# Optimization experiments

Hardware: AMD Instinct MI355X
Metric: run time of the kernel (lower is better)

## Reference

```python
import jax, jax.numpy as jnp
import numpy as np

B, C, H, W = 2, 512, 30, 40
K = 64
PATCH, STRIDE = 4, 1
EPS = 1e-12  # torch F.normalize eps


def _l2norm(v, axis):
    n = jnp.sqrt(jnp.sum(v * v, axis=axis, keepdims=True))
    return v / jnp.maximum(n, EPS)


def setup_inputs() -> dict:
    key = jax.random.key(0)
    k1, k2, k3 = jax.random.split(key, 3)
    x = jax.random.normal(k1, (B, C, H, W), dtype=jnp.float32)
    conv_w = jax.random.normal(k2, (K, C), dtype=jnp.float32) * 0.05  # 1x1 conv weight, no bias (vlad_v2=False)
    centroids = jax.random.normal(k3, (K, C), dtype=jnp.float32)
    return {"x": x, "conv_w": conv_w, "centroids": centroids}


def reference(x, conv_w, centroids):
    b, c, h, w = x.shape
    k = centroids.shape[0]
    # input L2 normalization along channels
    xn = _l2norm(x, axis=1)
    # soft assignment: 1x1 conv + softmax over clusters
    soft = jax.nn.softmax(jnp.einsum('kc,bchw->bkhw', conv_w, xn), axis=1)
    # weighted residuals [B,K,C,H,W] (fused; original loops over K)
    resid = (xn[:, None, :, :, :] - centroids[None, :, :, None, None]) * soft[:, :, None, :, :]
    # global VLAD: sum over spatial
    vlad_global = jnp.sum(resid, axis=(-2, -1))  # [B,K,C]
    vlad_global = _l2norm(vlad_global, axis=2).reshape(b, -1)
    vlad_global = _l2norm(vlad_global, axis=1)
    # integral image over [B, K*C, H, W]
    r = resid.reshape(b, k * c, h, w)
    integ = jnp.cumsum(jnp.cumsum(r, axis=-1), axis=-2)
    integ = jnp.pad(integ, ((0, 0), (0, 0), (1, 0), (1, 0)))  # [B,KC,H+1,W+1]
    # box-sum via integral-image differences (equiv. to the dilated 2x2 grouped conv)
    p, s = PATCH, STRIDE
    hp = (h - p) // s + 1
    wp = (w - p) // s + 1
    ye, xe = (hp - 1) * s + 1, (wp - 1) * s + 1
    tl = integ[:, :, 0:ye:s, 0:xe:s]
    tr = integ[:, :, 0:ye:s, p:p + xe:s]
    bl = integ[:, :, p:p + ye:s, 0:xe:s]
    br = integ[:, :, p:p + ye:s, p:p + xe:s]
    box = (br - tr - bl + tl) / (p * p)  # [B,KC,hp,wp]
    v = box.reshape(b, k, c, hp * wp)
    v = _l2norm(v, axis=2)  # intra-cluster norm
    v = v.reshape(b, k * c, hp * wp)
    vlad_local = _l2norm(v, axis=1)  # [B, K*C, hp*wp]
    return (vlad_local, vlad_global)
```

## Files before the change

### kernel.cpp

```cpp
#include <hip/hip_runtime.h>
#include <math.h>

#define BB 2
#define CC 512
#define HH 30
#define WW 40
#define KK 64
#define NPIX (HH*WW)
#define HP 27
#define WP 37
#define NP (HP*WP)
#define LEPS 1e-12f
#define NCG 16

__global__ __launch_bounds__(512) void k_norm_soft(
    const float* __restrict__ x, const float* __restrict__ convw,
    float* __restrict__ xn, float* __restrict__ soft)
{
  const int h = blockIdx.x, b = blockIdx.y;
  const int t = threadIdx.x;
  __shared__ float xc[64][41];
  __shared__ float cw[64][65];
  __shared__ float Lb[KK][WW + 1];
  __shared__ float psum[12][WW];
  __shared__ float invn[WW];
  __shared__ float mx[WW], Zs[WW];

  const size_t xbase = (size_t)b * CC * NPIX + (size_t)h * WW;

  if (t < 480) {
    const int w = t % 40, part = t / 40;
    float s = 0.f;
    for (int c = part; c < CC; c += 12) {
      const float v = x[xbase + (size_t)c * NPIX + w];
      s = fmaf(v, v, s);
    }
    psum[part][w] = s;
  }
  __syncthreads();
  if (t < 40) {
    float s = 0.f;
    #pragma unroll
    for (int p = 0; p < 12; ++p) s += psum[p][t];
    invn[t] = 1.f / fmaxf(sqrtf(s), LEPS);
  }
  __syncthreads();

  const int k = t & 63, wp = t >> 6;
  float acc[5] = {0.f, 0.f, 0.f, 0.f, 0.f};
  for (int cb = 0; cb < CC; cb += 64) {
    #pragma unroll
    for (int n = 0; n < 5; ++n) {
      const int idx = t + 512 * n;
      const int c = idx / 40, w = idx % 40;
      const float v = x[xbase + (size_t)(cb + c) * NPIX + w] * invn[w];
      xc[c][w] = v;
      xn[xbase + (size_t)(cb + c) * NPIX + w] = v;
    }
    #pragma unroll
    for (int n = 0; n < 8; ++n) {
      const int idx = t + 512 * n;
      const int kk2 = idx >> 6, c2 = idx & 63;
      cw[kk2][c2] = convw[(size_t)kk2 * CC + cb + c2];
    }
    __syncthreads();
    #pragma unroll 1
    for (int c = 0; c < 64; ++c) {
      const float cv = cw[k][c];
      #pragma unroll
      for (int n = 0; n < 5; ++n)
        acc[n] = fmaf(cv, xc[c][wp + 8 * n], acc[n]);
    }
    __syncthreads();
  }
  #pragma unroll
  for (int n = 0; n < 5; ++n) Lb[k][wp + 8 * n] = acc[n];
  __syncthreads();
  if (t < 40) {
    float m = -1e30f;
    for (int kk2 = 0; kk2 < KK; ++kk2) m = fmaxf(m, Lb[kk2][t]);
    float Z = 0.f;
    for (int kk2 = 0; kk2 < KK; ++kk2) Z += expf(Lb[kk2][t] - m);
    mx[t] = m; Zs[t] = Z;
  }
  __syncthreads();
  const size_t sbase = (size_t)b * KK * NPIX + (size_t)h * WW;
  #pragma unroll
  for (int n = 0; n < 5; ++n) {
    const int idx = t + 512 * n;
    const int kk2 = idx / 40, w = idx % 40;
    soft[sbase + (size_t)kk2 * NPIX + w] = expf(Lb[kk2][w] - mx[w]) / Zs[w];
  }
}

__global__ __launch_bounds__(256) void k_global(
    const float* __restrict__ xn, const float* __restrict__ soft,
    const float* __restrict__ cent, float* __restrict__ ghat)
{
  const int k = blockIdx.x, b = blockIdx.y, t = threadIdx.x;
  __shared__ float sb[NPIX];
  __shared__ float red[256];
  const float* srow = soft + ((size_t)b * KK + k) * NPIX;
  for (int i2 = t; i2 < NPIX; i2 += 256) sb[i2] = srow[i2];
  __syncthreads();
  float p = 0.f;
  for (int i2 = t; i2 < NPIX; i2 += 256) p += sb[i2];
  red[t] = p;
  __syncthreads();
  for (int s = 128; s > 0; s >>= 1) { if (t < s) red[t] += red[t + s]; __syncthreads(); }
  const float Sg = red[0];
  __syncthreads();

  const int c0 = t, c1 = t + 256;
  const float* x0 = xn + ((size_t)b * CC + c0) * NPIX;
  const float* x1 = xn + ((size_t)b * CC + c1) * NPIX;
  float a0 = 0.f, a1 = 0.f;
  for (int p4 = 0; p4 < NPIX; p4 += 4) {
    const float4 s4 = *(const float4*)&sb[p4];
    const float4 v0 = *(const float4*)(x0 + p4);
    const float4 v1 = *(const float4*)(x1 + p4);
    a0 = fmaf(s4.x, v0.x, a0); a0 = fmaf(s4.y, v0.y, a0);
    a0 = fmaf(s4.z, v0.z, a0); a0 = fmaf(s4.w, v0.w, a0);
    a1 = fmaf(s4.x, v1.x, a1); a1 = fmaf(s4.y, v1.y, a1);
    a1 = fmaf(s4.z, v1.z, a1); a1 = fmaf(s4.w, v1.w, a1);
  }
  const float g0 = a0 - cent[(size_t)k * CC + c0] * Sg;
  const float g1 = a1 - cent[(size_t)k * CC + c1] * Sg;
  red[t] = g0 * g0 + g1 * g1;
  __syncthreads();
  for (int s = 128; s > 0; s >>= 1) { if (t < s) red[t] += red[t + s]; __syncthreads(); }
  const float inv = 1.f / fmaxf(sqrtf(red[0]), LEPS);
  float* gr = ghat + ((size_t)b * KK + k) * CC;
  gr[c0] = g0 * inv; gr[c1] = g1 * inv;
}

__global__ __launch_bounds__(256) void k_global2(
    const float* __restrict__ ghat, float* __restrict__ outg)
{
  const int b = blockIdx.x, t = threadIdx.x;
  __shared__ float red[256];
  const float* gb = ghat + (size_t)b * KK * CC;
  float p = 0.f;
  for (int i2 = t; i2 < KK * CC; i2 += 256) { const float v = gb[i2]; p = fmaf(v, v, p); }
  red[t] = p;
  __syncthreads();
  for (int s = 128; s > 0; s >>= 1) { if (t < s) red[t] += red[t + s]; __syncthreads(); }
  const float inv = 1.f / fmaxf(sqrtf(red[0]), LEPS);
  for (int i2 = t; i2 < KK * CC; i2 += 256)
    outg[(size_t)b * KK * CC + i2] = gb[i2] * inv;
}

template<int PHASE>
__global__ __launch_bounds__(320, 3) void k_local4(
    const float* __restrict__ xn, const float* __restrict__ soft,
    const float* __restrict__ cent, float* __restrict__ sp,
    const float* __restrict__ fs, float* __restrict__ out)
{
  const int cg = blockIdx.x;
  const int kg = blockIdx.y;
  const int bz = blockIdx.z;
  const int b = bz / 7, iq = bz % 7;
  const int i0 = iq * 4;
  const int n_i = (iq == 6) ? 3 : 4;
  const int k0 = kg * 4, c0 = cg * 32;
  const int t = threadIdx.x;

  __shared__ float xn_l[32][280];
  __shared__ float soft_l[4][280];
  __shared__ float cent_l[4][32];

  for (int u = t; u < 2240; u += 320) {
    const int c = u / 70, rem = u % 70;
    const int rl = rem / 10, q = rem % 10;
    int row = i0 + rl; if (row > HH - 1) row = HH - 1;
    *(float4*)&xn_l[c][rl * 40 + q * 4] =
      *(const float4*)&xn[((size_t)(b * CC + c0 + c)) * NPIX + (size_t)row * 40 + q * 4];
  }
  if (t < 280) {
    const int kk = t / 70, rem = t % 70;
    const int rl = rem / 10, q = rem % 10;
    int row = i0 + rl; if (row > HH - 1) row = HH - 1;
    *(float4*)&soft_l[kk][rl * 40 + q * 4] =
      *(const float4*)&soft[((size_t)(b * KK + k0 + kk)) * NPIX + (size_t)row * 40 + q * 4];
  }
  if (t < 128) cent_l[t >> 5][t & 31] = cent[(size_t)(k0 + (t >> 5)) * CC + c0 + (t & 31)];
  __syncthreads();

  const int c8 = (PHASE == 0) ? (t & 7) : (t / 40);
  const int j  = (PHASE == 0) ? (t >> 3) : (t % 40);

  for (int ii = 0; ii < n_i; ++ii) {
    const int i = i0 + ii;
    float acc[4][4];
    float Ssum[4] = {0.f, 0.f, 0.f, 0.f};
    #pragma unroll
    for (int cc = 0; cc < 4; ++cc)
      #pragma unroll
      for (int kk = 0; kk < 4; ++kk) acc[cc][kk] = 0.f;

    #pragma unroll
    for (int r = 0; r < 4; ++r) {
      const int base = (ii + r) * 40 + j;
      float sv[4][4], xv[4][4];
      #pragma unroll
      for (int kk = 0; kk < 4; ++kk)
        #pragma unroll
        for (int dx = 0; dx < 4; ++dx) sv[kk][dx] = soft_l[kk][base + dx];
      #pragma unroll
      for (int cc = 0; cc < 4; ++cc)
        #pragma unroll
        for (int dx = 0; dx < 4; ++dx) xv[cc][dx] = xn_l[cc * 8 + c8][base + dx];
      #pragma unroll
      for (int kk = 0; kk < 4; ++kk)
        Ssum[kk] += (sv[kk][0] + sv[kk][1]) + (sv[kk][2] + sv[kk][3]);
      #pragma unroll
      for (int cc = 0; cc < 4; ++cc)
        #pragma unroll
        for (int kk = 0; kk < 4; ++kk) {
          float a = acc[cc][kk];
          a = fmaf(xv[cc][0], sv[kk][0], a);
          a = fmaf(xv[cc][1], sv[kk][1], a);
          a = fmaf(xv[cc][2], sv[kk][2], a);
          a = fmaf(xv[cc][3], sv[kk][3], a);
          acc[cc][kk] = a;
        }
    }

    if (PHASE == 0) {
      #pragma unroll
      for (int kk = 0; kk < 4; ++kk) {
        float s = 0.f;
        #pragma unroll
        for (int cc = 0; cc < 4; ++cc) {
          const float raw = fmaf(-cent_l[kk][cc * 8 + c8], Ssum[kk], acc[cc][kk]);
          s = fmaf(raw, raw, s);
        }
        s += __shfl_xor(s, 1, 64);
        s += __shfl_xor(s, 2, 64);
        s += __shfl_xor(s, 4, 64);
        if (c8 == 0 && j < WP)
          sp[(((size_t)(b * KK + k0 + kk)) * NCG + cg) * NP + (size_t)i * WP + j] = s;
      }
    } else if (j < WP) {
      float fsv[4];
      #pragma unroll
      for (int kk = 0; kk < 4; ++kk)
        fsv[kk] = fs[((size_t)(b * KK + k0 + kk)) * NP + (size_t)i * WP + j];
      #pragma unroll
      for (int kk = 0; kk < 4; ++kk)
        #pragma unroll
        for (int cc = 0; cc < 4; ++cc) {
          const float raw = fmaf(-cent_l[kk][cc * 8 + c8], Ssum[kk], acc[cc][kk]);
          out[((size_t)((b * KK + k0 + kk) * CC + c0 + cc * 8 + c8)) * NP
              + (size_t)i * WP + j] = raw * fsv[kk];
        }
    }
  }
}

__global__ __launch_bounds__(256) void k_nf(
    const float* __restrict__ sp, float* __restrict__ fs)
{
  const int b = blockIdx.y, t = threadIdx.x;
  const int k = t >> 2, dp = t & 3;
  const int p = blockIdx.x * 4 + dp;
  __shared__ float red[64][4];
  __shared__ float inv2s[4];
  const bool ok = p < NP;
  float sr = 0.f;
  if (ok) {
    #pragma unroll
    for (int g = 0; g < NCG; ++g)
      sr += sp[(((size_t)(b * KK + k)) * NCG + g) * NP + p];
  }
  const float iv = 1.f / fmaxf(sqrtf(sr) * 0.0625f, LEPS);
  red[k][dp] = sr * (1.f / 256.f) * iv * iv;
  __syncthreads();
  if (t < 4) {
    float s = 0.f;
    #pragma unroll
    for (int kk = 0; kk < 64; ++kk) s += red[kk][t];
    inv2s[t] = 1.f / fmaxf(sqrtf(s), LEPS);
  }
  __syncthreads();
  if (ok)
    fs[((size_t)(b * KK + k)) * NP + p] = 0.0625f * iv * inv2s[dp];
}

extern "C" void kernel_launch(void* const* d_in, const int* in_sizes, int n_in,
                              void* d_out, int out_size, void* d_ws, size_t ws_size,
                              hipStream_t stream)
{
  const float* x     = (const float*)d_in[0];
  const float* convw = (const float*)d_in[1];
  const float* cent  = (const float*)d_in[2];
  float* out = (float*)d_out;
  float* ws  = (float*)d_ws;

  float* xn   = ws;
  float* soft = xn   + (size_t)BB * CC * NPIX;
  float* fs   = soft + (size_t)BB * KK * NPIX;
  float* ghat = fs   + (size_t)BB * KK * NP;
  float* sp   = ghat + (size_t)BB * KK * CC;

  k_norm_soft<<<dim3(HH, BB), 512, 0, stream>>>(x, convw, xn, soft);
  k_global<<<dim3(KK, BB), 256, 0, stream>>>(xn, soft, cent, ghat);
  k_global2<<<dim3(BB), 256, 0, stream>>>(ghat, out + (size_t)BB * KK * CC * NP);
  k_local4<0><<<dim3(NCG, KK / 4, BB * 7), 320, 0, stream>>>(xn, soft, cent, sp, fs, out);
  k_nf<<<dim3((NP + 3) / 4, BB), 256, 0, stream>>>(sp, fs);
  k_local4<1><<<dim3(NCG, KK / 4, BB * 7), 320, 0, stream>>>(xn, soft, cent, sp, fs, out);
}
```

Before: 442.3 us.

## Register-block local box-sum kernel over 4 output columns and split global norm

The local VLAD kernel is restructured so each thread computes a 4-wide strip of output columns for one row, using float4 shared-memory loads with a padded row stride. This reuses loaded x and soft values across the overlapping 4x4 windows. The soft-assignment window sums are now computed once per block into shared memory instead of being recomputed by every channel thread. The single-block global L2 normalization is split into a reduction kernel and a grid-wide scaling kernel, which spreads the 32K-element write across many blocks. The cost is higher register pressure (64 accumulators per thread), and the PHASE 1 stores become strided per thread, which may reduce write coalescing.

```diff
diff --git a/kernel.cpp b/kernel.cpp
--- a/kernel.cpp
+++ b/kernel.cpp
@@ -12,6 +12,7 @@
 #define NP (HP*WP)
 #define LEPS 1e-12f
 #define NCG 16
+#define XSTR 292
 
 __global__ __launch_bounds__(512) void k_norm_soft(
     const float* __restrict__ x, const float* __restrict__ convw,
@@ -134,8 +135,8 @@
   gr[c0] = g0 * inv; gr[c1] = g1 * inv;
 }
 
-__global__ __launch_bounds__(256) void k_global2(
-    const float* __restrict__ ghat, float* __restrict__ outg)
+__global__ __launch_bounds__(256) void k_g2a(
+    const float* __restrict__ ghat, float* __restrict__ inv2g)
 {
   const int b = blockIdx.x, t = threadIdx.x;
   __shared__ float red[256];
@@ -145,13 +146,21 @@
   red[t] = p;
   __syncthreads();
   for (int s = 128; s > 0; s >>= 1) { if (t < s) red[t] += red[t + s]; __syncthreads(); }
-  const float inv = 1.f / fmaxf(sqrtf(red[0]), LEPS);
-  for (int i2 = t; i2 < KK * CC; i2 += 256)
-    outg[(size_t)b * KK * CC + i2] = gb[i2] * inv;
+  if (t == 0) inv2g[b] = 1.f / fmaxf(sqrtf(red[0]), LEPS);
+}
+
+__global__ __launch_bounds__(256) void k_g2b(
+    const float* __restrict__ ghat, const float* __restrict__ inv2g,
+    float* __restrict__ outg)
+{
+  const int b = blockIdx.y;
+  const int u = blockIdx.x * 256 + threadIdx.x;
+  if (u < KK * CC)
+    outg[(size_t)b * KK * CC + u] = ghat[(size_t)b * KK * CC + u] * inv2g[b];
 }
 
 template<int PHASE>
-__global__ __launch_bounds__(320, 3) void k_local4(
+__global__ __launch_bounds__(320, 3) void k_local5(
     const float* __restrict__ xn, const float* __restrict__ soft,
     const float* __restrict__ cent, float* __restrict__ sp,
     const float* __restrict__ fs, float* __restrict__ out)
@@ -161,99 +170,137 @@
   const int bz = blockIdx.z;
   const int b = bz / 7, iq = bz % 7;
   const int i0 = iq * 4;
-  const int n_i = (iq == 6) ? 3 : 4;
   const int k0 = kg * 4, c0 = cg * 32;
   const int t = threadIdx.x;
-
-  __shared__ float xn_l[32][280];
-  __shared__ float soft_l[4][280];
+  const int c4 = t & 7;
+  const int jq = (t >> 3) % 10;
+  const int i2 = t / 80;
+  const int j0 = jq * 4;
+  const int i = i0 + i2;
+
+  __shared__ float xn_l[32 * XSTR];
+  __shared__ float soft_l[4 * XSTR];
+  __shared__ float S_l[4][4][48];
   __shared__ float cent_l[4][32];
 
   for (int u = t; u < 2240; u += 320) {
-    const int c = u / 70, rem = u % 70;
-    const int rl = rem / 10, q = rem % 10;
+    const int c = u / 70, rem = u - c * 70;
+    const int rl = rem / 10, q = rem - rl * 10;
     int row = i0 + rl; if (row > HH - 1) row = HH - 1;
-    *(float4*)&xn_l[c][rl * 40 + q * 4] =
+    *(float4*)&xn_l[c * XSTR + rl * 40 + q * 4] =
       *(const float4*)&xn[((size_t)(b * CC + c0 + c)) * NPIX + (size_t)row * 40 + q * 4];
   }
   if (t < 280) {
-    const int kk = t / 70, rem = t % 70;
-    const int rl = rem / 10, q = rem % 10;
+    const int kk = t / 70, rem = t - kk * 70;
+    const int rl = rem / 10, q = rem - rl * 10;
     int row = i0 + rl; if (row > HH - 1) row = HH - 1;
-    *(float4*)&soft_l[kk][rl * 40 + q * 4] =
+    *(float4*)&soft_l[kk * XSTR + rl * 40 + q * 4] =
       *(const float4*)&soft[((size_t)(b * KK + k0 + kk)) * NPIX + (size_t)row * 40 + q * 4];
   }
   if (t < 128) cent_l[t >> 5][t & 31] = cent[(size_t)(k0 + (t >> 5)) * CC + c0 + (t & 31)];
   __syncthreads();
 
-  const int c8 = (PHASE == 0) ? (t & 7) : (t / 40);
-  const int j  = (PHASE == 0) ? (t >> 3) : (t % 40);
-
-  for (int ii = 0; ii < n_i; ++ii) {
-    const int i = i0 + ii;
-    float acc[4][4];
-    float Ssum[4] = {0.f, 0.f, 0.f, 0.f};
-    #pragma unroll
-    for (int cc = 0; cc < 4; ++cc)
-      #pragma unroll
-      for (int kk = 0; kk < 4; ++kk) acc[cc][kk] = 0.f;
-
-    #pragma unroll
-    for (int r = 0; r < 4; ++r) {
-      const int base = (ii + r) * 40 + j;
-      float sv[4][4], xv[4][4];
+  if (t < 160) {
+    const int kk = t / 40, j = t - kk * 40;
+    #pragma unroll
+    for (int ii = 0; ii < 4; ++ii) {
+      float s = 0.f;
+      #pragma unroll
+      for (int r = 0; r < 4; ++r) {
+        const int base = kk * XSTR + (ii + r) * 40 + j;
+        s += (soft_l[base] + soft_l[base + 1]) + (soft_l[base + 2] + soft_l[base + 3]);
+      }
+      S_l[kk][ii][j] = s;
+    }
+  }
+  __syncthreads();
+
+  float acc[4][4][4];
+  #pragma unroll
+  for (int cc = 0; cc < 4; ++cc)
+    #pragma unroll
+    for (int kk = 0; kk < 4; ++kk)
+      #pragma unroll
+      for (int jd = 0; jd < 4; ++jd) acc[cc][kk][jd] = 0.f;
+
+  #pragma unroll
+  for (int r = 0; r < 4; ++r) {
+    const int rbase = (i2 + r) * 40 + j0;
+    float sw[4][8];
+    #pragma unroll
+    for (int kk = 0; kk < 4; ++kk) {
+      const float4 s0 = *(const float4*)&soft_l[kk * XSTR + rbase];
+      const float4 s1 = *(const float4*)&soft_l[kk * XSTR + rbase + 4];
+      sw[kk][0] = s0.x; sw[kk][1] = s0.y; sw[kk][2] = s0.z; sw[kk][3] = s0.w;
+      sw[kk][4] = s1.x; sw[kk][5] = s1.y; sw[kk][6] = s1.z; sw[kk][7] = s1.w;
+    }
+    #pragma unroll
+    for (int cc = 0; cc < 4; ++cc) {
+      const int cr = (cc * 8 + c4) * XSTR + rbase;
+      const float4 x0 = *(const float4*)&xn_l[cr];
+      const float4 x1 = *(const float4*)&xn_l[cr + 4];
+      const float xw[8] = {x0.x, x0.y, x0.z, x0.w, x1.x, x1.y, x1.z, x1.w};
       #pragma unroll
       for (int kk = 0; kk < 4; ++kk)
         #pragma unroll
-        for (int dx = 0; dx < 4; ++dx) sv[kk][dx] = soft_l[kk][base + dx];
-      #pragma unroll
-      for (int cc = 0; cc < 4; ++cc)
-        #pragma unroll
-        for (int dx = 0; dx < 4; ++dx) xv[cc][dx] = xn_l[cc * 8 + c8][base + dx];
-      #pragma unroll
-      for (int kk = 0; kk < 4; ++kk)
-        Ssum[kk] += (sv[kk][0] + sv[kk][1]) + (sv[kk][2] + sv[kk][3]);
-      #pragma unroll
-      for (int cc = 0; cc < 4; ++cc)
-        #pragma unroll
-        for (int kk = 0; kk < 4; ++kk) {
-          float a = acc[cc][kk];
-          a = fmaf(xv[cc][0], sv[kk][0], a);
-          a = fmaf(xv[cc][1], sv[kk][1], a);
-          a = fmaf(xv[cc][2], sv[kk][2], a);
-          a = fmaf(xv[cc][3], sv[kk][3], a);
-          acc[cc][kk] = a;
+        for (int jd = 0; jd < 4; ++jd) {
+          float a = acc[cc][kk][jd];
+          a = fmaf(xw[jd + 0], sw[kk][jd + 0], a);
+          a = fmaf(xw[jd + 1], sw[kk][jd + 1], a);
+          a = fmaf(xw[jd + 2], sw[kk][jd + 2], a);
+          a = fmaf(xw[jd + 3], sw[kk][jd + 3], a);
+          acc[cc][kk][jd] = a;
         }
     }
-
-    if (PHASE == 0) {
-      #pragma unroll
-      for (int kk = 0; kk < 4; ++kk) {
+  }
+
+  if (PHASE == 0) {
+    #pragma unroll
+    for (int kk = 0; kk < 4; ++kk) {
+      const float4 Sq = *(const float4*)&S_l[kk][i2][j0];
+      const float Sv[4] = {Sq.x, Sq.y, Sq.z, Sq.w};
+      float sq[4];
+      #pragma unroll
+      for (int jd = 0; jd < 4; ++jd) {
         float s = 0.f;
         #pragma unroll
         for (int cc = 0; cc < 4; ++cc) {
-          const float raw = fmaf(-cent_l[kk][cc * 8 + c8], Ssum[kk], acc[cc][kk]);
+          const float raw = fmaf(-cent_l[kk][cc * 8 + c4], Sv[jd], acc[cc][kk][jd]);
           s = fmaf(raw, raw, s);
         }
         s += __shfl_xor(s, 1, 64);
         s += __shfl_xor(s, 2, 64);
         s += __shfl_xor(s, 4, 64);
-        if (c8 == 0 && j < WP)
-          sp[(((size_t)(b * KK + k0 + kk)) * NCG + cg) * NP + (size_t)i * WP + j] = s;
+        sq[jd] = s;
       }
-    } else if (j < WP) {
+      if (c4 == 0 && i < HP) {
+        #pragma unroll
+        for (int jd = 0; jd < 4; ++jd)
+          if (j0 + jd < WP)
+            sp[(((size_t)(b * KK + k0 + kk)) * NCG + cg) * NP + (size_t)i * WP + j0 + jd] = sq[jd];
+      }
+    }
+  } else if (i < HP) {
+    #pragma unroll
+    for (int kk = 0; kk < 4; ++kk) {
+      const float4 Sq = *(const float4*)&S_l[kk][i2][j0];
+      const float Sv[4] = {Sq.x, Sq.y, Sq.z, Sq.w};
       float fsv[4];
       #pragma unroll
-      for (int kk = 0; kk < 4; ++kk)
-        fsv[kk] = fs[((size_t)(b * KK + k0 + kk)) * NP + (size_t)i * WP + j];
-      #pragma unroll
-      for (int kk = 0; kk < 4; ++kk)
+      for (int jd = 0; jd < 4; ++jd)
+        fsv[jd] = (j0 + jd < WP)
+          ? fs[((size_t)(b * KK + k0 + kk)) * NP + (size_t)i * WP + j0 + jd] : 0.f;
+      #pragma unroll
+      for (int cc = 0; cc < 4; ++cc) {
+        const int c = c0 + cc * 8 + c4;
         #pragma unroll
-        for (int cc = 0; cc < 4; ++cc) {
-          const float raw = fmaf(-cent_l[kk][cc * 8 + c8], Ssum[kk], acc[cc][kk]);
-          out[((size_t)((b * KK + k0 + kk) * CC + c0 + cc * 8 + c8)) * NP
-              + (size_t)i * WP + j] = raw * fsv[kk];
-        }
+        for (int jd = 0; jd < 4; ++jd)
+          if (j0 + jd < WP) {
+            const float raw = fmaf(-cent_l[kk][cc * 8 + c4], Sv[jd], acc[cc][kk][jd]);
+            out[((size_t)((b * KK + k0 + kk) * CC + c)) * NP + (size_t)i * WP + j0 + jd]
+              = raw * fsv[jd];
+          }
+      }
     }
   }
 }
@@ -297,16 +344,20 @@
   float* out = (float*)d_out;
   float* ws  = (float*)d_ws;
 
-  float* xn   = ws;
-  float* soft = xn   + (size_t)BB * CC * NPIX;
-  float* fs   = soft + (size_t)BB * KK * NPIX;
-  float* ghat = fs   + (size_t)BB * KK * NP;
-  float* sp   = ghat + (size_t)BB * KK * CC;
+  float* xn    = ws;
+  float* soft  = xn    + (size_t)BB * CC * NPIX;
+  float* fs    = soft  + (size_t)BB * KK * NPIX;
+  float* ghat  = fs    + (size_t)BB * KK * NP;
+  float* sp    = ghat  + (size_t)BB * KK * CC;
+  float* inv2g = sp    + (size_t)BB * KK * NCG * NP;
+
+  float* outg = out + (size_t)BB * KK * CC * NP;
 
   k_norm_soft<<<dim3(HH, BB), 512, 0, stream>>>(x, convw, xn, soft);
   k_global<<<dim3(KK, BB), 256, 0, stream>>>(xn, soft, cent, ghat);
-  k_global2<<<dim3(BB), 256, 0, stream>>>(ghat, out + (size_t)BB * KK * CC * NP);
-  k_local4<0><<<dim3(NCG, KK / 4, BB * 7), 320, 0, stream>>>(xn, soft, cent, sp, fs, out);
+  k_g2a<<<dim3(BB), 256, 0, stream>>>(ghat, inv2g);
+  k_g2b<<<dim3((KK * CC + 255) / 256, BB), 256, 0, stream>>>(ghat, inv2g, outg);
+  k_local5<0><<<dim3(NCG, KK / 4, BB * 7), 320, 0, stream>>>(xn, soft, cent, sp, fs, out);
   k_nf<<<dim3((NP + 3) / 4, BB), 256, 0, stream>>>(sp, fs);
-  k_local4<1><<<dim3(NCG, KK / 4, BB * 7), 320, 0, stream>>>(xn, soft, cent, sp, fs, out);
-}
+  k_local5<1><<<dim3(NCG, KK / 4, BB * 7), 320, 0, stream>>>(xn, soft, cent, sp, fs, out);
+}
```

Result: slower. 981.6 us (+121.9%).
